# Kernel tuning notes

Measured on AMD Instinct MI355X. Metric: run time of the kernel, lower is better.

The kernel has to match this reference:

```python
import jax, jax.numpy as jnp
import numpy as np

B = 131072
EPS = 1e-5

def _attn(x, Wq, Wk, Wv, Wo):
    # x: (B, 10, 1); Wq/Wk/Wv: (1, 16); Wo: (16, 1)
    Q = x @ Wq  # (B, 10, 16)
    K = x @ Wk
    V = x @ Wv
    A = jnp.einsum('bqd,bkd->bqk', Q, K) / 4.0  # sqrt(16) = 4
    A = jax.nn.softmax(A, axis=1)  # NOTE: torch Softmax(dim=1) -> axis 1, not -1
    out = jnp.einsum('bqk,bkd->bqd', A, V) @ Wo  # (B, 10, 1)
    return out[..., 0]  # squeeze -> (B, 10)

def _bn(h, gamma, beta):
    # BatchNorm1d training-mode math (batch stats, biased variance)
    mu = jnp.mean(h, axis=0)
    var = jnp.mean(jnp.square(h - mu), axis=0)
    return gamma * (h - mu) * jax.lax.rsqrt(var + EPS) + beta

def setup_inputs() -> dict:
    key = jax.random.key(0)
    ks = jax.random.split(key, 24)
    n = lambda k, shp, s=1.0: (jax.random.normal(k, shp, dtype=jnp.float32) * s)
    inp = {
        'x':   n(ks[0], (B, 10, 1)),
        'Wq1': n(ks[1], (1, 16)), 'Wk1': n(ks[2], (1, 16)),
        'Wv1': n(ks[3], (1, 16)), 'Wo1': n(ks[4], (16, 1)),
        'Wq2': n(ks[5], (1, 16)), 'Wk2': n(ks[6], (1, 16)),
        'Wv2': n(ks[7], (1, 16)), 'Wo2': n(ks[8], (16, 1)),
        # layer1: Linear(10,128) BN ReLU Linear(128,256) BN ReLU Linear(256,10)
        'W1a': n(ks[9], (10, 128), 0.3), 'b1a': jnp.zeros((128,), jnp.float32),
        'g1a': jnp.ones((128,), jnp.float32), 'be1a': jnp.zeros((128,), jnp.float32),
        'W1b': n(ks[10], (128, 256), 0.09), 'b1b': jnp.zeros((256,), jnp.float32),
        'g1b': jnp.ones((256,), jnp.float32), 'be1b': jnp.zeros((256,), jnp.float32),
        'W1c': n(ks[11], (256, 10), 0.06), 'b1c': jnp.zeros((10,), jnp.float32),
        # layer2: Linear(10,128) BN ReLU Linear(128,256) BN ReLU Linear(256,2)
        'W2a': n(ks[12], (10, 128), 0.3), 'b2a': jnp.zeros((128,), jnp.float32),
        'g2a': jnp.ones((128,), jnp.float32), 'be2a': jnp.zeros((128,), jnp.float32),
        'W2b': n(ks[13], (128, 256), 0.09), 'b2b': jnp.zeros((256,), jnp.float32),
        'g2b': jnp.ones((256,), jnp.float32), 'be2b': jnp.zeros((256,), jnp.float32),
        'W2c': n(ks[14], (256, 2), 0.06), 'b2c': jnp.zeros((2,), jnp.float32),
    }
    return inp

def reference(x, Wq1, Wk1, Wv1, Wo1, Wq2, Wk2, Wv2, Wo2,
              W1a, b1a, g1a, be1a, W1b, b1b, g1b, be1b, W1c, b1c,
              W2a, b2a, g2a, be2a, W2b, b2b, g2b, be2b, W2c, b2c):
    h = _attn(x, Wq1, Wk1, Wv1, Wo1)                 # (B, 10)
    h = jax.nn.relu(_bn(h @ W1a + b1a, g1a, be1a))   # (B, 128)
    h = jax.nn.relu(_bn(h @ W1b + b1b, g1b, be1b))   # (B, 256)
    h = h @ W1c + b1c                                # (B, 10)
    h = _attn(h[..., None], Wq2, Wk2, Wv2, Wo2)      # (B, 10)
    h = jax.nn.relu(_bn(h @ W2a + b2a, g2a, be2a))   # (B, 128)
    h = jax.nn.relu(_bn(h @ W2b + b2b, g2b, be2b))   # (B, 256)
    return h @ W2c + b2c                             # (B, 2)
```

## Files before the change

### kernel.cpp

```cpp
#include <hip/hip_runtime.h>
#include <hip/hip_bf16.h>

#define EPS 1e-5f
constexpr int BN = 131072;
constexpr int NBKT = 32;

typedef __attribute__((ext_vector_type(8))) short bf16x8;
typedef __attribute__((ext_vector_type(4))) float f32x4;

constexpr size_t OFF_H   = 0;
constexpr size_t OFF_HH  = OFF_H  + (size_t)BN*10;
constexpr size_t OFF_M1  = OFF_HH + (size_t)BN*10;
constexpr size_t OFF_S2  = OFF_M1 + 65;
constexpr size_t OFF_M3  = OFF_S2 + 512;
constexpr size_t OFF_S4  = OFF_M3 + 65;
constexpr size_t OFF_WA1 = OFF_S4 + 512;
constexpr size_t OFF_BA1 = OFF_WA1 + 1280;
constexpr size_t OFF_WA2 = OFF_BA1 + 128;
constexpr size_t OFF_BA2 = OFF_WA2 + 1280;
constexpr size_t OFF_SC2 = OFF_BA2 + 128;
constexpr size_t OFF_TC2 = OFF_SC2 + 256;
constexpr size_t OFF_SC4 = OFF_TC2 + 256;
constexpr size_t OFF_TC4 = OFF_SC4 + 256;
constexpr size_t OFF_WB1 = OFF_TC4 + 256;
constexpr size_t OFF_BB1 = OFF_WB1 + 32768;
constexpr size_t OFF_WB2 = OFF_BB1 + 256;
constexpr size_t OFF_BB2 = OFF_WB2 + 32768;
constexpr size_t OFF_P1  = OFF_BB2 + 256;
constexpr size_t OFF_P3  = OFF_P1 + 512*65;
constexpr size_t OFF_S2B = OFF_P3 + 512*65;
constexpr size_t OFF_S4B = OFF_S2B + (size_t)NBKT*512;
constexpr size_t OFF_WT1 = OFF_S4B + (size_t)NBKT*512;
constexpr size_t OFF_WT2 = OFF_WT1 + 16384;
constexpr size_t OFF_END = OFF_WT2 + 16384;
constexpr size_t OFF_Z_BYTES = ((OFF_END*4 + 255) & ~(size_t)255);
constexpr size_t WS_NEED_OLD  = OFF_Z_BYTES + (size_t)BN*256*2;
constexpr size_t WS_NEED_MFMA = WS_NEED_OLD;

__device__ __forceinline__ float wsum(float v){
  v += __shfl_down(v, 32);
  v += __shfl_down(v, 16);
  v += __shfl_down(v, 8);
  v += __shfl_down(v, 4);
  v += __shfl_down(v, 2);
  v += __shfl_down(v, 1);
  return v;
}

__device__ __forceinline__ unsigned pk_bf16(float a, float b){
  union { __hip_bfloat16 h[2]; unsigned u; } cv;
  cv.h[0] = __float2bfloat16(a);
  cv.h[1] = __float2bfloat16(b);
  return cv.u;
}

__device__ __forceinline__ unsigned short bf16_1(float a){
  union { __hip_bfloat16 h; unsigned short u; } cv;
  cv.h = __float2bfloat16(a);
  return cv.u;
}

__device__ __forceinline__ void attn10(const float* xr, float cqk, float cvo, float* y){
  #pragma unroll
  for (int q=0;q<10;q++) y[q] = 0.f;
  #pragma unroll
  for (int k=0;k<10;k++){
    float t = cqk * xr[k];
    float m = t*xr[0];
    #pragma unroll
    for (int q=1;q<10;q++) m = fmaxf(m, t*xr[q]);
    float ex[10]; float s = 0.f;
    #pragma unroll
    for (int q=0;q<10;q++){ ex[q] = __expf(t*xr[q]-m); s += ex[q]; }
    float f = xr[k]/s;
    #pragma unroll
    for (int q=0;q<10;q++) y[q] += ex[q]*f;
  }
  #pragma unroll
  for (int q=0;q<10;q++) y[q] *= cvo;
}

__device__ __forceinline__ void moments_block(const float* y, float (*red)[65],
                                              float* Pb, int t){
  int lane = t & 63, w = t >> 6;
  #pragma unroll
  for (int i=0;i<10;i++){
    float v = wsum(y[i]);
    if (lane==0) red[w][i] = v;
  }
  #pragma unroll
  for (int i=0;i<10;i++){
    #pragma unroll
    for (int j=i;j<10;j++){
      float v = wsum(y[i]*y[j]);
      if (lane==0) red[w][10 + 10*i - i*(i-1)/2 + (j-i)] = v;
    }
  }
  __syncthreads();
  if (t < 65)
    Pb[(size_t)blockIdx.x*65 + t] = red[0][t]+red[1][t]+red[2][t]+red[3][t];
}

__device__ __forceinline__ void moments10(const float* y, float* M, int lane){
  #pragma unroll
  for (int i=0;i<10;i++){
    float s = wsum(y[i]);
    if (lane==0) atomicAdd(&M[i], s);
  }
  #pragma unroll
  for (int i=0;i<10;i++){
    #pragma unroll
    for (int j=i;j<10;j++){
      int id = 10*i - i*(i-1)/2 + (j-i);
      float s = wsum(y[i]*y[j]);
      if (lane==0) atomicAdd(&M[10+id], s);
    }
  }
}

__global__ __launch_bounds__(256) void k_attn_in(
    const float* __restrict__ x,
    const float* __restrict__ Wq, const float* __restrict__ Wk,
    const float* __restrict__ Wv, const float* __restrict__ Wo,
    float* __restrict__ h, float* __restrict__ Pb){
  __shared__ float red[4][65];
  int t = threadIdx.x;
  size_t b = (size_t)blockIdx.x*256 + t;
  float cqk=0.f, cvo=0.f;
  #pragma unroll
  for (int d=0;d<16;d++){ cqk += Wq[d]*Wk[d]; cvo += Wv[d]*Wo[d]; }
  cqk *= 0.25f;
  float xr[10];
  #pragma unroll
  for (int q=0;q<10;q++) xr[q] = x[b*10+q];
  float y[10];
  attn10(xr, cqk, cvo, y);
  #pragma unroll
  for (int q=0;q<10;q++) h[b*10+q] = y[q];
  moments_block(y, red, Pb, t);
}

__global__ void k_fold10_part(const float* __restrict__ Pb,
                              const float* __restrict__ W,
                              const float* __restrict__ bv, const float* __restrict__ g,
                              const float* __restrict__ be,
                              float* __restrict__ WT, float* __restrict__ bo){
  __shared__ float sM[65];
  int t = threadIdx.x;
  if (t < 65){
    float acc = 0.f;
    for (int gg=0; gg<512; gg++) acc += Pb[(size_t)gg*65 + t];
    sM[t] = acc;
  }
  __syncthreads();
  int j = t;
  if (j >= 128) return;
  const float invB = 1.f/(float)BN;
  float Eh[10];
  #pragma unroll
  for (int i=0;i<10;i++) Eh[i] = sM[i]*invB;
  float wj[10];
  #pragma unroll
  for (int i=0;i<10;i++) wj[i] = W[i*128+j];
  float mu = bv[j];
  #pragma unroll
  for (int i=0;i<10;i++) mu += Eh[i]*wj[i];
  float var = 0.f;
  #pragma unroll
  for (int i=0;i<10;i++){
    #pragma unroll
    for (int l=0;l<10;l++){
      int a = i<l ? i : l, c = i<l ? l : i;
      int id = 10*a - a*(a-1)/2 + (c-a);
      float cov = sM[10+id]*invB - Eh[i]*Eh[l];
      var += wj[i]*wj[l]*cov;
    }
  }
  float s = g[j]*rsqrtf(var + EPS);
  #pragma unroll
  for (int i=0;i<10;i++) WT[j*10+i] = wj[i]*s;
  bo[j] = (bv[j]-mu)*s + be[j];
}

__global__ void k_fold10_atomic(const float* __restrict__ M,
                                const float* __restrict__ W,
                                const float* __restrict__ bv, const float* __restrict__ g,
                                const float* __restrict__ be,
                                float* __restrict__ WT, float* __restrict__ bo){
  int j = threadIdx.x;
  if (j >= 128) return;
  const float invB = 1.f/(float)BN;
  float Eh[10];
  #pragma unroll
  for (int i=0;i<10;i++) Eh[i] = M[i]*invB;
  float wj[10];
  #pragma unroll
  for (int i=0;i<10;i++) wj[i] = W[i*128+j];
  float mu = bv[j];
  #pragma unroll
  for (int i=0;i<10;i++) mu += Eh[i]*wj[i];
  float var = 0.f;
  #pragma unroll
  for (int i=0;i<10;i++){
    #pragma unroll
    for (int l=0;l<10;l++){
      int a = i<l ? i : l, c = i<l ? l : i;
      int id = 10*a - a*(a-1)/2 + (c-a);
      float cov = M[10+id]*invB - Eh[i]*Eh[l];
      var += wj[i]*wj[l]*cov;
    }
  }
  float s = g[j]*rsqrtf(var + EPS);
  #pragma unroll
  for (int i=0;i<10;i++) WT[j*10+i] = wj[i]*s;
  bo[j] = (bv[j]-mu)*s + be[j];
}

__global__ void k_fold_affine(const float* __restrict__ stats,
                              const float* __restrict__ g,
                              const float* __restrict__ be,
                              float* __restrict__ s, float* __restrict__ tt){
  int j = threadIdx.x;
  if (j >= 256) return;
  float su = 0.f, sq = 0.f;
  #pragma unroll 4
  for (int k=0;k<NBKT;k++){
    su += stats[k*512 + j];
    sq += stats[k*512 + 256 + j];
  }
  const float invB = 1.f/(float)BN;
  float mu  = su*invB;
  float var = sq*invB - mu*mu;
  float sc = g[j]*rsqrtf(var + EPS);
  s[j]  = sc;
  tt[j] = be[j] - mu*sc;
}

__global__ __launch_bounds__(256) void k_prep_wt(const float* __restrict__ W,
                                                 unsigned short* __restrict__ WT){
  int idx = blockIdx.x*256 + threadIdx.x;
  int c = idx >> 7, k = idx & 127;
  WT[idx] = bf16_1(W[k*256 + c]);
}

__global__ __launch_bounds__(256) void k_layer_mfma(
    const float* __restrict__ h,
    const float* __restrict__ WaT,
    const float* __restrict__ ba,
    const unsigned short* __restrict__ WT,
    const float* __restrict__ bb,
    unsigned short* __restrict__ z,
    float* __restrict__ stats)
{
  __shared__ unsigned short h1s[64*128];
  __shared__ float hs[64][10];
  __shared__ float sWaT[1280];
  __shared__ float sstats[512];
  int t = threadIdx.x;
  int lane = t & 63, w = t >> 6;
  int ci = lane & 15, g = lane >> 4;
  size_t row0 = (size_t)blockIdx.x * 64;

  bf16x8 bfr[4][4];
  #pragma unroll
  for (int nt=0; nt<4; nt++)
    #pragma unroll
    for (int kt=0; kt<4; kt++){
      union { uint4 u; bf16x8 v; } cv;
      cv.u = *(const uint4*)(WT + (size_t)(w*64 + nt*16 + ci)*128 + kt*32 + g*8);
      bfr[nt][kt] = cv.v;
    }

  for (int idx = t; idx < 640; idx += 256) hs[idx/10][idx%10] = h[row0*10 + idx];
  for (int idx = t; idx < 1280; idx += 256) sWaT[idx] = WaT[idx];
  __syncthreads();

  {
    int r = lane;
    int i0 = w * 32;
    float hr[10];
    #pragma unroll
    for (int l=0;l<10;l++) hr[l] = hs[r][l];
    #pragma unroll
    for (int j=0;j<4;j++){
      unsigned pk[4];
      #pragma unroll
      for (int q=0;q<4;q++){
        int i = i0 + j*8 + q*2;
        float v0 = ba[i], v1 = ba[i+1];
        #pragma unroll
        for (int l=0;l<10;l++){
          v0 = fmaf(hr[l], sWaT[i*10+l],     v0);
          v1 = fmaf(hr[l], sWaT[(i+1)*10+l], v1);
        }
        pk[q] = pk_bf16(fmaxf(v0,0.f), fmaxf(v1,0.f));
      }
      int byte = r*256 + (((i0 + j*8)*2) ^ ((r&7)<<4));
      *(uint4*)((char*)h1s + byte) = make_uint4(pk[0],pk[1],pk[2],pk[3]);
    }
  }
  __syncthreads();

  f32x4 acc[4][4];
  #pragma unroll
  for (int mt=0;mt<4;mt++)
    #pragma unroll
    for (int nt=0;nt<4;nt++)
      acc[mt][nt] = (f32x4){0.f,0.f,0.f,0.f};

  #pragma unroll
  for (int mt=0; mt<4; mt++){
    int r = mt*16 + ci;
    bf16x8 af[4];
    #pragma unroll
    for (int kt=0; kt<4; kt++){
      int byte = r*256 + ((kt*64 + g*16) ^ ((r&7)<<4));
      af[kt] = *(const bf16x8*)((const char*)h1s + byte);
    }
    #pragma unroll
    for (int nt=0; nt<4; nt++)
      #pragma unroll
      for (int kt=0; kt<4; kt++)
        acc[mt][nt] = __builtin_amdgcn_mfma_f32_16x16x32_bf16(
            af[kt], bfr[nt][kt], acc[mt][nt], 0, 0, 0);
  }

  float bbv[4];
  #pragma unroll
  for (int nt=0;nt<4;nt++) bbv[nt] = bb[w*64 + nt*16 + ci];
  float csum[4] = {0,0,0,0}, csq[4] = {0,0,0,0};
  #pragma unroll
  for (int mt=0; mt<4; mt++){
    #pragma unroll
    for (int nt=0; nt<4; nt++){
      #pragma unroll
      for (int j=0;j<4;j++){
        float zv = acc[mt][nt][j] + bbv[nt];
        int r = mt*16 + g*4 + j;
        int c = w*64 + nt*16 + ci;
        z[(row0 + r)*256 + c] = bf16_1(zv);
        csum[nt] += zv;
        csq[nt]  += zv*zv;
      }
    }
  }
  #pragma unroll
  for (int nt=0; nt<4; nt++){
    float s1 = csum[nt], s2 = csq[nt];
    s1 += __shfl_down(s1, 32); s1 += __shfl_down(s1, 16);
    s2 += __shfl_down(s2, 32); s2 += __shfl_down(s2, 16);
    if (lane < 16){
      sstats[w*64 + nt*16 + ci]       = s1;
      sstats[256 + w*64 + nt*16 + ci] = s2;
    }
  }
  __syncthreads();
  int bkt = blockIdx.x & (NBKT-1);
  atomicAdd(&stats[bkt*512 + t], sstats[t]);
  atomicAdd(&stats[bkt*512 + 256 + t], sstats[256+t]);
}

__global__ __launch_bounds__(256) void k_layer_big(
    const float* __restrict__ h,
    const float* __restrict__ WaT,
    const float* __restrict__ ba,
    const float* __restrict__ Wb,
    const float* __restrict__ bb,
    unsigned short* __restrict__ z,
    float* __restrict__ stats)
{
  __shared__ float h1T[128][68];
  __shared__ float hs[64][10];
  __shared__ float sWaT[1280];
  __shared__ float sstats[512];
  int t = threadIdx.x;
  size_t row0 = (size_t)blockIdx.x * 64;

  for (int idx = t; idx < 640; idx += 256) hs[idx/10][idx%10] = h[row0*10 + idx];
  for (int idx = t; idx < 1280; idx += 256) sWaT[idx] = WaT[idx];
  sstats[t] = 0.f; sstats[256+t] = 0.f;
  __syncthreads();
  {
    int r  = t & 63;
    int i0 = (t >> 6) * 32;
    float hr[10];
    #pragma unroll
    for (int l=0;l<10;l++) hr[l] = hs[r][l];
    for (int k=0;k<32;k++){
      int i = i0 + k;
      float v = ba[i];
      #pragma unroll
      for (int l=0;l<10;l++) v = fmaf(hr[l], sWaT[i*10+l], v);
      h1T[i][r] = fmaxf(v, 0.f);
    }
  }
  __syncthreads();
  int tx = t & 15;
  int ty = t >> 4;
  float acc[4][16];
  #pragma unroll
  for (int r=0;r<4;r++)
    #pragma unroll
    for (int c=0;c<16;c++) acc[r][c] = 0.f;
  const float* __restrict__ wrow = Wb + tx*16;
  for (int i=0;i<128;i++){
    const float4* wp = (const float4*)(wrow + (size_t)i*256);
    float wv[16];
    #pragma unroll
    for (int q=0;q<4;q++){
      float4 w = wp[q];
      wv[4*q+0]=w.x; wv[4*q+1]=w.y; wv[4*q+2]=w.z; wv[4*q+3]=w.w;
    }
    float4 av = *(const float4*)&h1T[i][ty*4];
    float a4[4] = {av.x, av.y, av.z, av.w};
    #pragma unroll
    for (int r=0;r<4;r++)
      #pragma unroll
      for (int c=0;c<16;c++)
        acc[r][c] = fmaf(a4[r], wv[c], acc[r][c]);
  }
  #pragma unroll
  for (int r=0;r<4;r++){
    unsigned p[8];
    #pragma unroll
    for (int q=0;q<8;q++){
      float z0 = acc[r][2*q]   + bb[tx*16 + 2*q];
      float z1 = acc[r][2*q+1] + bb[tx*16 + 2*q+1];
      acc[r][2*q]   = z0;
      acc[r][2*q+1] = z1;
      p[q] = pk_bf16(z0, z1);
    }
    uint4* zp = (uint4*)(z + (row0 + ty*4 + r)*256 + tx*16);
    zp[0] = make_uint4(p[0],p[1],p[2],p[3]);
    zp[1] = make_uint4(p[4],p[5],p[6],p[7]);
  }
  int lane = t & 63;
  #pragma unroll
  for (int c=0;c<16;c++){
    float s1 = acc[0][c]+acc[1][c]+acc[2][c]+acc[3][c];
    float q1 = acc[0][c]*acc[0][c]+acc[1][c]*acc[1][c]
             + acc[2][c]*acc[2][c]+acc[3][c]*acc[3][c];
    s1 += __shfl_down(s1, 32); s1 += __shfl_down(s1, 16);
    q1 += __shfl_down(q1, 32); q1 += __shfl_down(q1, 16);
    if (lane < 16){
      atomicAdd(&sstats[tx*16+c], s1);
      atomicAdd(&sstats[256+tx*16+c], q1);
    }
  }
  __syncthreads();
  int bkt = blockIdx.x & (NBKT-1);
  atomicAdd(&stats[bkt*512 + t], sstats[t]);
  atomicAdd(&stats[bkt*512 + 256 + t], sstats[256+t]);
}

__global__ __launch_bounds__(256) void k_consume_mid(
    const unsigned short* __restrict__ z,
    const float* __restrict__ s_g, const float* __restrict__ t_g,
    const float* __restrict__ Wc,  const float* __restrict__ bc,
    const float* __restrict__ Wq, const float* __restrict__ Wk,
    const float* __restrict__ Wv, const float* __restrict__ Wo,
    float* __restrict__ hh, float* __restrict__ Pb){
  __shared__ float sW[2560];
  __shared__ float ss[256], st[256];
  __shared__ float red[4][65];
  int t = threadIdx.x;
  for (int idx=t; idx<2560; idx+=256) sW[idx] = Wc[idx];
  ss[t] = s_g[t]; st[t] = t_g[t];
  __syncthreads();
  size_t b = (size_t)blockIdx.x*256 + t;
  float z3[10];
  #pragma unroll
  for (int l=0;l<10;l++) z3[l] = bc[l];
  const uint4* zr = (const uint4*)(z + b*256);
  for (int v=0; v<32; v++){
    uint4 pkt = zr[v];
    unsigned w4[4] = {pkt.x, pkt.y, pkt.z, pkt.w};
    #pragma unroll
    for (int q=0;q<4;q++){
      int j = v*8 + q*2;
      float f0 = __uint_as_float(w4[q] << 16);
      float f1 = __uint_as_float(w4[q] & 0xffff0000u);
      float h20 = fmaxf(fmaf(ss[j],   f0, st[j]),   0.f);
      float h21 = fmaxf(fmaf(ss[j+1], f1, st[j+1]), 0.f);
      #pragma unroll
      for (int l=0;l<10;l++) z3[l] = fmaf(h20, sW[j*10+l], z3[l]);
      #pragma unroll
      for (int l=0;l<10;l++) z3[l] = fmaf(h21, sW[(j+1)*10+l], z3[l]);
    }
  }
  float cqk=0.f, cvo=0.f;
  #pragma unroll
  for (int d=0;d<16;d++){ cqk += Wq[d]*Wk[d]; cvo += Wv[d]*Wo[d]; }
  cqk *= 0.25f;
  float y[10];
  attn10(z3, cqk, cvo, y);
  #pragma unroll
  for (int q=0;q<10;q++) hh[b*10+q] = y[q];
  moments_block(y, red, Pb, t);
}

__global__ __launch_bounds__(256) void k_consume_out(
    const unsigned short* __restrict__ z,
    const float* __restrict__ s_g, const float* __restrict__ t_g,
    const float* __restrict__ Wc,  const float* __restrict__ bc,
    float* __restrict__ out){
  __shared__ float sW0[256], sW1[256], ss[256], st[256];
  int t = threadIdx.x;
  sW0[t] = Wc[t*2]; sW1[t] = Wc[t*2+1];
  ss[t] = s_g[t]; st[t] = t_g[t];
  __syncthreads();
  size_t b = (size_t)blockIdx.x*256 + t;
  float o0 = bc[0], o1 = bc[1];
  const uint4* zr = (const uint4*)(z + b*256);
  for (int v=0; v<32; v++){
    uint4 pkt = zr[v];
    unsigned w4[4] = {pkt.x, pkt.y, pkt.z, pkt.w};
    #pragma unroll
    for (int q=0;q<4;q++){
      int j = v*8 + q*2;
      float f0 = __uint_as_float(w4[q] << 16);
      float f1 = __uint_as_float(w4[q] & 0xffff0000u);
      float h20 = fmaxf(fmaf(ss[j],   f0, st[j]),   0.f);
      float h21 = fmaxf(fmaf(ss[j+1], f1, st[j+1]), 0.f);
      o0 = fmaf(h20, sW0[j],   o0); o1 = fmaf(h20, sW1[j],   o1);
      o0 = fmaf(h21, sW0[j+1], o0); o1 = fmaf(h21, sW1[j+1], o1);
    }
  }
  out[b*2]   = o0;
  out[b*2+1] = o1;
}

__global__ void k_fold_big(const float* __restrict__ stats,
                           const float* __restrict__ W,
                           const float* __restrict__ bv, const float* __restrict__ g,
                           const float* __restrict__ be,
                           float* __restrict__ Wf, float* __restrict__ bf){
  int j = blockIdx.x*256 + threadIdx.x;
  if (j >= 256) return;
  const float invB = 1.f/(float)BN;
  float mu  = stats[j]*invB;
  float var = stats[256+j]*invB - mu*mu;
  float s = g[j]*rsqrtf(var + EPS);
  bf[j] = (bv[j]-mu)*s + be[j];
  for (int i=0;i<128;i++) Wf[i*256+j] = W[i*256+j]*s;
}

__global__ __launch_bounds__(256) void k_mid(
    const float* __restrict__ h,
    const float* __restrict__ WaT, const float* __restrict__ ba,
    const float* __restrict__ Wb,  const float* __restrict__ bb,
    float* __restrict__ stats){
  int b = blockIdx.x*256 + threadIdx.x;
  if (b >= BN) return;
  float hr[10];
  #pragma unroll
  for (int l=0;l<10;l++) hr[l] = h[(size_t)b*10+l];
  int lane = threadIdx.x & 63;
  for (int jc=0;jc<4;jc++){
    float acc[64];
    #pragma unroll
    for (int j=0;j<64;j++) acc[j] = bb[jc*64+j];
    for (int i=0;i<128;i++){
      float h1 = ba[i];
      #pragma unroll
      for (int l=0;l<10;l++) h1 += hr[l]*WaT[i*10+l];
      h1 = fmaxf(h1, 0.f);
      const float* __restrict__ w = &Wb[i*256 + jc*64];
      #pragma unroll
      for (int j=0;j<64;j++) acc[j] += h1*w[j];
    }
    #pragma unroll
    for (int j=0;j<64;j++){
      float s1 = wsum(acc[j]);
      float s2 = wsum(acc[j]*acc[j]);
      if (lane==0){
        atomicAdd(&stats[jc*64+j], s1);
        atomicAdd(&stats[256+jc*64+j], s2);
      }
    }
  }
}

__global__ __launch_bounds__(256) void k_mid2(
    const float* __restrict__ h,
    const float* __restrict__ WaT, const float* __restrict__ ba,
    const float* __restrict__ Wbf, const float* __restrict__ bbf,
    const float* __restrict__ Wc,  const float* __restrict__ bc,
    const float* __restrict__ Wq, const float* __restrict__ Wk,
    const float* __restrict__ Wv, const float* __restrict__ Wo,
    float* __restrict__ hh, float* __restrict__ M){
  int b = blockIdx.x*256 + threadIdx.x;
  if (b >= BN) return;
  float hr[10];
  #pragma unroll
  for (int l=0;l<10;l++) hr[l] = h[(size_t)b*10+l];
  float z3[10];
  #pragma unroll
  for (int l=0;l<10;l++) z3[l] = bc[l];
  for (int jc=0;jc<4;jc++){
    float acc[64];
    #pragma unroll
    for (int j=0;j<64;j++) acc[j] = bbf[jc*64+j];
    for (int i=0;i<128;i++){
      float h1 = ba[i];
      #pragma unroll
      for (int l=0;l<10;l++) h1 += hr[l]*WaT[i*10+l];
      h1 = fmaxf(h1, 0.f);
      const float* __restrict__ w = &Wbf[i*256 + jc*64];
      #pragma unroll
      for (int j=0;j<64;j++) acc[j] += h1*w[j];
    }
    #pragma unroll
    for (int j=0;j<64;j++){
      float h2 = fmaxf(acc[j], 0.f);
      const float* __restrict__ wc = &Wc[(jc*64+j)*10];
      #pragma unroll
      for (int l=0;l<10;l++) z3[l] += h2*wc[l];
    }
  }
  float cqk=0.f, cvo=0.f;
  #pragma unroll
  for (int d=0;d<16;d++){ cqk += Wq[d]*Wk[d]; cvo += Wv[d]*Wo[d]; }
  cqk *= 0.25f;
  float y[10];
  attn10(z3, cqk, cvo, y);
  #pragma unroll
  for (int q=0;q<10;q++) hh[(size_t)b*10+q] = y[q];
  moments10(y, M, threadIdx.x & 63);
}

__global__ __launch_bounds__(256) void k_out(
    const float* __restrict__ h,
    const float* __restrict__ WaT, const float* __restrict__ ba,
    const float* __restrict__ Wbf, const float* __restrict__ bbf,
    const float* __restrict__ Wc,  const float* __restrict__ bc,
    float* __restrict__ out){
  int b = blockIdx.x*256 + threadIdx.x;
  if (b >= BN) return;
  float hr[10];
  #pragma unroll
  for (int l=0;l<10;l++) hr[l] = h[(size_t)b*10+l];
  float o0 = bc[0], o1 = bc[1];
  for (int jc=0;jc<4;jc++){
    float acc[64];
    #pragma unroll
    for (int j=0;j<64;j++) acc[j] = bbf[jc*64+j];
    for (int i=0;i<128;i++){
      float h4 = ba[i];
      #pragma unroll
      for (int l=0;l<10;l++) h4 += hr[l]*WaT[i*10+l];
      h4 = fmaxf(h4, 0.f);
      const float* __restrict__ w = &Wbf[i*256 + jc*64];
      #pragma unroll
      for (int j=0;j<64;j++) acc[j] += h4*w[j];
    }
    #pragma unroll
    for (int j=0;j<64;j++){
      float h5 = fmaxf(acc[j], 0.f);
      o0 += h5*Wc[(jc*64+j)*2];
      o1 += h5*Wc[(jc*64+j)*2+1];
    }
  }
  out[(size_t)b*2]   = o0;
  out[(size_t)b*2+1] = o1;
}

extern "C" void kernel_launch(void* const* d_in, const int* in_sizes, int n_in,
                              void* d_out, int out_size, void* d_ws, size_t ws_size,
                              hipStream_t stream){
  const float* x   = (const float*)d_in[0];
  const float* Wq1 = (const float*)d_in[1];
  const float* Wk1 = (const float*)d_in[2];
  const float* Wv1 = (const float*)d_in[3];
  const float* Wo1 = (const float*)d_in[4];
  const float* Wq2 = (const float*)d_in[5];
  const float* Wk2 = (const float*)d_in[6];
  const float* Wv2 = (const float*)d_in[7];
  const float* Wo2 = (const float*)d_in[8];
  const float* W1a = (const float*)d_in[9];  const float* b1a = (const float*)d_in[10];
  const float* g1a = (const float*)d_in[11]; const float* be1a= (const float*)d_in[12];
  const float* W1b = (const float*)d_in[13]; const float* b1b = (const float*)d_in[14];
  const float* g1b = (const float*)d_in[15]; const float* be1b= (const float*)d_in[16];
  const float* W1c = (const float*)d_in[17]; const float* b1c = (const float*)d_in[18];
  const float* W2a = (const float*)d_in[19]; const float* b2a = (const float*)d_in[20];
  const float* g2a = (const float*)d_in[21]; const float* be2a= (const float*)d_in[22];
  const float* W2b = (const float*)d_in[23]; const float* b2b = (const float*)d_in[24];
  const float* g2b = (const float*)d_in[25]; const float* be2b= (const float*)d_in[26];
  const float* W2c = (const float*)d_in[27]; const float* b2c = (const float*)d_in[28];

  float* f   = (float*)d_ws;
  float* h   = f + OFF_H;
  float* hh  = f + OFF_HH;
  float* M1  = f + OFF_M1;
  float* S2  = f + OFF_S2;
  float* M3  = f + OFF_M3;
  float* S4  = f + OFF_S4;
  float* WA1 = f + OFF_WA1; float* BA1 = f + OFF_BA1;
  float* WA2 = f + OFF_WA2; float* BA2 = f + OFF_BA2;
  float* SC2 = f + OFF_SC2; float* TC2 = f + OFF_TC2;
  float* SC4 = f + OFF_SC4; float* TC4 = f + OFF_TC4;
  float* WB1 = f + OFF_WB1; float* BB1 = f + OFF_BB1;
  float* WB2 = f + OFF_WB2; float* BB2 = f + OFF_BB2;
  float* P1  = f + OFF_P1;  float* P3  = f + OFF_P3;
  float* S2B = f + OFF_S2B; float* S4B = f + OFF_S4B;
  unsigned short* WT1 = (unsigned short*)(f + OFF_WT1);
  unsigned short* WT2 = (unsigned short*)(f + OFF_WT2);
  unsigned short* Z = (unsigned short*)((char*)d_ws + OFF_Z_BYTES);

  dim3 grid(BN/256), blk(256);

  if (ws_size >= WS_NEED_MFMA){
    hipMemsetAsync(S2B, 0, (size_t)2*NBKT*512*sizeof(float), stream);
    dim3 gbig(BN/64);
    k_prep_wt<<<128,blk,0,stream>>>(W1b, WT1);
    k_prep_wt<<<128,blk,0,stream>>>(W2b, WT2);
    k_attn_in<<<grid,blk,0,stream>>>(x, Wq1,Wk1,Wv1,Wo1, h, P1);
    k_fold10_part<<<1,128,0,stream>>>(P1, W1a,b1a,g1a,be1a, WA1,BA1);
    k_layer_mfma<<<gbig,blk,0,stream>>>(h, WA1,BA1, WT1,b1b, Z, S2B);
    k_fold_affine<<<1,256,0,stream>>>(S2B, g1b, be1b, SC2, TC2);
    k_consume_mid<<<grid,blk,0,stream>>>(Z, SC2,TC2, W1c,b1c, Wq2,Wk2,Wv2,Wo2, hh, P3);
    k_fold10_part<<<1,128,0,stream>>>(P3, W2a,b2a,g2a,be2a, WA2,BA2);
    k_layer_mfma<<<gbig,blk,0,stream>>>(hh, WA2,BA2, WT2,b2b, Z, S4B);
    k_fold_affine<<<1,256,0,stream>>>(S4B, g2b, be2b, SC4, TC4);
    k_consume_out<<<grid,blk,0,stream>>>(Z, SC4,TC4, W2c,b2c, (float*)d_out);
  } else {
    hipMemsetAsync(M1, 0, (65+512+65+512)*sizeof(float), stream);
    k_attn_in<<<grid,blk,0,stream>>>(x, Wq1,Wk1,Wv1,Wo1, h, P1);
    k_fold10_part<<<1,128,0,stream>>>(P1, W1a,b1a,g1a,be1a, WA1,BA1);
    k_mid<<<grid,blk,0,stream>>>(h, WA1,BA1, W1b,b1b, S2);
    k_fold_big<<<1,256,0,stream>>>(S2, W1b,b1b,g1b,be1b, WB1,BB1);
    k_mid2<<<grid,blk,0,stream>>>(h, WA1,BA1, WB1,BB1, W1c,b1c, Wq2,Wk2,Wv2,Wo2, hh, M3);
    k_fold10_atomic<<<1,128,0,stream>>>(M3, W2a,b2a,g2a,be2a, WA2,BA2);
    k_mid<<<grid,blk,0,stream>>>(hh, WA2,BA2, W2b,b2b, S4);
    k_fold_big<<<1,256,0,stream>>>(S4, W2b,b2b,g2b,be2b, WB2,BB2);
    k_out<<<grid,blk,0,stream>>>(hh, WA2,BA2, WB2,BB2, W2c,b2c, (float*)d_out);
  }
}
```

Baseline: 225.9 us.

## Store bf16 intermediate column-major and split consumer rows across thread pairs

Result: no change. 228.9 us (+1.3%).

```diff
diff --git a/kernel.cpp b/kernel.cpp
--- a/kernel.cpp
+++ b/kernel.cpp
@@ -27,15 +27,14 @@
 constexpr size_t OFF_WB2 = OFF_BB1 + 256;
 constexpr size_t OFF_BB2 = OFF_WB2 + 32768;
 constexpr size_t OFF_P1  = OFF_BB2 + 256;
-constexpr size_t OFF_P3  = OFF_P1 + 512*65;
-constexpr size_t OFF_S2B = OFF_P3 + 512*65;
+constexpr size_t OFF_P3  = OFF_P1 + 1024*65;
+constexpr size_t OFF_S2B = OFF_P3 + 1024*65;
 constexpr size_t OFF_S4B = OFF_S2B + (size_t)NBKT*512;
 constexpr size_t OFF_WT1 = OFF_S4B + (size_t)NBKT*512;
 constexpr size_t OFF_WT2 = OFF_WT1 + 16384;
 constexpr size_t OFF_END = OFF_WT2 + 16384;
 constexpr size_t OFF_Z_BYTES = ((OFF_END*4 + 255) & ~(size_t)255);
-constexpr size_t WS_NEED_OLD  = OFF_Z_BYTES + (size_t)BN*256*2;
-constexpr size_t WS_NEED_MFMA = WS_NEED_OLD;
+constexpr size_t WS_NEED = OFF_Z_BYTES + (size_t)256*BN*2;
 
 __device__ __forceinline__ float wsum(float v){
   v += __shfl_down(v, 32);
@@ -81,7 +80,7 @@
 }
 
 __device__ __forceinline__ void moments_block(const float* y, float (*red)[65],
-                                              float* Pb, int t){
+                                              float* Pb, int t, float scale){
   int lane = t & 63, w = t >> 6;
   #pragma unroll
   for (int i=0;i<10;i++){
@@ -98,7 +97,7 @@
   }
   __syncthreads();
   if (t < 65)
-    Pb[(size_t)blockIdx.x*65 + t] = red[0][t]+red[1][t]+red[2][t]+red[3][t];
+    Pb[(size_t)blockIdx.x*65 + t] = (red[0][t]+red[1][t]+red[2][t]+red[3][t])*scale;
 }
 
 __device__ __forceinline__ void moments10(const float* y, float* M, int lane){
@@ -123,34 +122,49 @@
     const float* __restrict__ Wq, const float* __restrict__ Wk,
     const float* __restrict__ Wv, const float* __restrict__ Wo,
     float* __restrict__ h, float* __restrict__ Pb){
+  __shared__ float xs[256][11];
   __shared__ float red[4][65];
   int t = threadIdx.x;
-  size_t b = (size_t)blockIdx.x*256 + t;
+  size_t base = (size_t)blockIdx.x*2560;
+  for (int idx=t; idx<2560; idx+=256) xs[idx/10][idx%10] = x[base+idx];
   float cqk=0.f, cvo=0.f;
   #pragma unroll
   for (int d=0;d<16;d++){ cqk += Wq[d]*Wk[d]; cvo += Wv[d]*Wo[d]; }
   cqk *= 0.25f;
+  __syncthreads();
   float xr[10];
   #pragma unroll
-  for (int q=0;q<10;q++) xr[q] = x[b*10+q];
+  for (int q=0;q<10;q++) xr[q] = xs[t][q];
   float y[10];
   attn10(xr, cqk, cvo, y);
   #pragma unroll
-  for (int q=0;q<10;q++) h[b*10+q] = y[q];
-  moments_block(y, red, Pb, t);
-}
-
-__global__ void k_fold10_part(const float* __restrict__ Pb,
+  for (int q=0;q<10;q++) xs[t][q] = y[q];
+  moments_block(y, red, Pb, t, 1.0f);
+  for (int idx=t; idx<2560; idx+=256) h[base+idx] = xs[idx/10][idx%10];
+}
+
+__global__ void k_fold10_part(const float* __restrict__ Pb, int npart,
                               const float* __restrict__ W,
                               const float* __restrict__ bv, const float* __restrict__ g,
                               const float* __restrict__ be,
                               float* __restrict__ WT, float* __restrict__ bo){
+  __shared__ float part[65][8];
   __shared__ float sM[65];
   int t = threadIdx.x;
+  if (t < 520){
+    int c = t>>3, k = t&7;
+    int n = npart>>3;
+    float acc = 0.f;
+    #pragma unroll 4
+    for (int i=0;i<n;i++) acc += Pb[(size_t)(k*n+i)*65 + c];
+    part[c][k] = acc;
+  }
+  __syncthreads();
   if (t < 65){
-    float acc = 0.f;
-    for (int gg=0; gg<512; gg++) acc += Pb[(size_t)gg*65 + t];
-    sM[t] = acc;
+    float a = 0.f;
+    #pragma unroll
+    for (int k=0;k<8;k++) a += part[t][k];
+    sM[t] = a;
   }
   __syncthreads();
   int j = t;
@@ -236,9 +250,13 @@
   tt[j] = be[j] - mu*sc;
 }
 
-__global__ __launch_bounds__(256) void k_prep_wt(const float* __restrict__ W,
-                                                 unsigned short* __restrict__ WT){
-  int idx = blockIdx.x*256 + threadIdx.x;
+__global__ __launch_bounds__(256) void k_prep_wt2(
+    const float* __restrict__ W1, const float* __restrict__ W2,
+    unsigned short* __restrict__ WT1, unsigned short* __restrict__ WT2){
+  int g = blockIdx.x;
+  const float* W = (g < 128) ? W1 : W2;
+  unsigned short* WT = (g < 128) ? WT1 : WT2;
+  int idx = (g & 127)*256 + threadIdx.x;
   int c = idx >> 7, k = idx & 127;
   WT[idx] = bf16_1(W[k*256 + c]);
 }
@@ -249,13 +267,14 @@
     const float* __restrict__ ba,
     const unsigned short* __restrict__ WT,
     const float* __restrict__ bb,
-    unsigned short* __restrict__ z,
+    unsigned short* __restrict__ zt,
     float* __restrict__ stats)
 {
-  __shared__ unsigned short h1s[64*128];
-  __shared__ float hs[64][10];
+  __shared__ unsigned short zs[256*72];
+  __shared__ float hs[64][11];
   __shared__ float sWaT[1280];
   __shared__ float sstats[512];
+  unsigned short* h1s = zs;
   int t = threadIdx.x;
   int lane = t & 63, w = t >> 6;
   int ci = lane & 15, g = lane >> 4;
@@ -330,20 +349,16 @@
   for (int nt=0;nt<4;nt++) bbv[nt] = bb[w*64 + nt*16 + ci];
   float csum[4] = {0,0,0,0}, csq[4] = {0,0,0,0};
   #pragma unroll
-  for (int mt=0; mt<4; mt++){
-    #pragma unroll
-    for (int nt=0; nt<4; nt++){
+  for (int mt=0; mt<4; mt++)
+    #pragma unroll
+    for (int nt=0; nt<4; nt++)
       #pragma unroll
       for (int j=0;j<4;j++){
         float zv = acc[mt][nt][j] + bbv[nt];
-        int r = mt*16 + g*4 + j;
-        int c = w*64 + nt*16 + ci;
-        z[(row0 + r)*256 + c] = bf16_1(zv);
+        acc[mt][nt][j] = zv;
         csum[nt] += zv;
         csq[nt]  += zv*zv;
       }
-    }
-  }
   #pragma unroll
   for (int nt=0; nt<4; nt++){
     float s1 = csum[nt], s2 = csq[nt];
@@ -358,103 +373,31 @@
   int bkt = blockIdx.x & (NBKT-1);
   atomicAdd(&stats[bkt*512 + t], sstats[t]);
   atomicAdd(&stats[bkt*512 + 256 + t], sstats[256+t]);
-}
-
-__global__ __launch_bounds__(256) void k_layer_big(
-    const float* __restrict__ h,
-    const float* __restrict__ WaT,
-    const float* __restrict__ ba,
-    const float* __restrict__ Wb,
-    const float* __restrict__ bb,
-    unsigned short* __restrict__ z,
-    float* __restrict__ stats)
-{
-  __shared__ float h1T[128][68];
-  __shared__ float hs[64][10];
-  __shared__ float sWaT[1280];
-  __shared__ float sstats[512];
-  int t = threadIdx.x;
-  size_t row0 = (size_t)blockIdx.x * 64;
-
-  for (int idx = t; idx < 640; idx += 256) hs[idx/10][idx%10] = h[row0*10 + idx];
-  for (int idx = t; idx < 1280; idx += 256) sWaT[idx] = WaT[idx];
-  sstats[t] = 0.f; sstats[256+t] = 0.f;
-  __syncthreads();
-  {
-    int r  = t & 63;
-    int i0 = (t >> 6) * 32;
-    float hr[10];
-    #pragma unroll
-    for (int l=0;l<10;l++) hr[l] = hs[r][l];
-    for (int k=0;k<32;k++){
-      int i = i0 + k;
-      float v = ba[i];
-      #pragma unroll
-      for (int l=0;l<10;l++) v = fmaf(hr[l], sWaT[i*10+l], v);
-      h1T[i][r] = fmaxf(v, 0.f);
-    }
-  }
-  __syncthreads();
-  int tx = t & 15;
-  int ty = t >> 4;
-  float acc[4][16];
-  #pragma unroll
-  for (int r=0;r<4;r++)
-    #pragma unroll
-    for (int c=0;c<16;c++) acc[r][c] = 0.f;
-  const float* __restrict__ wrow = Wb + tx*16;
-  for (int i=0;i<128;i++){
-    const float4* wp = (const float4*)(wrow + (size_t)i*256);
-    float wv[16];
-    #pragma unroll
-    for (int q=0;q<4;q++){
-      float4 w = wp[q];
-      wv[4*q+0]=w.x; wv[4*q+1]=w.y; wv[4*q+2]=w.z; wv[4*q+3]=w.w;
-    }
-    float4 av = *(const float4*)&h1T[i][ty*4];
-    float a4[4] = {av.x, av.y, av.z, av.w};
-    #pragma unroll
-    for (int r=0;r<4;r++)
-      #pragma unroll
-      for (int c=0;c<16;c++)
-        acc[r][c] = fmaf(a4[r], wv[c], acc[r][c]);
-  }
-  #pragma unroll
-  for (int r=0;r<4;r++){
-    unsigned p[8];
-    #pragma unroll
-    for (int q=0;q<8;q++){
-      float z0 = acc[r][2*q]   + bb[tx*16 + 2*q];
-      float z1 = acc[r][2*q+1] + bb[tx*16 + 2*q+1];
-      acc[r][2*q]   = z0;
-      acc[r][2*q+1] = z1;
-      p[q] = pk_bf16(z0, z1);
-    }
-    uint4* zp = (uint4*)(z + (row0 + ty*4 + r)*256 + tx*16);
-    zp[0] = make_uint4(p[0],p[1],p[2],p[3]);
-    zp[1] = make_uint4(p[4],p[5],p[6],p[7]);
-  }
-  int lane = t & 63;
-  #pragma unroll
-  for (int c=0;c<16;c++){
-    float s1 = acc[0][c]+acc[1][c]+acc[2][c]+acc[3][c];
-    float q1 = acc[0][c]*acc[0][c]+acc[1][c]*acc[1][c]
-             + acc[2][c]*acc[2][c]+acc[3][c]*acc[3][c];
-    s1 += __shfl_down(s1, 32); s1 += __shfl_down(s1, 16);
-    q1 += __shfl_down(q1, 32); q1 += __shfl_down(q1, 16);
-    if (lane < 16){
-      atomicAdd(&sstats[tx*16+c], s1);
-      atomicAdd(&sstats[256+tx*16+c], q1);
-    }
-  }
-  __syncthreads();
-  int bkt = blockIdx.x & (NBKT-1);
-  atomicAdd(&stats[bkt*512 + t], sstats[t]);
-  atomicAdd(&stats[bkt*512 + 256 + t], sstats[256+t]);
+
+  #pragma unroll
+  for (int mt=0; mt<4; mt++)
+    #pragma unroll
+    for (int nt=0; nt<4; nt++){
+      int c = w*64 + nt*16 + ci;
+      int r0 = mt*16 + g*4;
+      uint2 v;
+      v.x = pk_bf16(acc[mt][nt][0], acc[mt][nt][1]);
+      v.y = pk_bf16(acc[mt][nt][2], acc[mt][nt][3]);
+      *(uint2*)&zs[c*72 + r0] = v;
+    }
+  __syncthreads();
+
+  #pragma unroll
+  for (int pass=0; pass<8; pass++){
+    int c  = (t>>3) + pass*32;
+    int rc = (t&7)*8;
+    uint4 v = *(const uint4*)&zs[c*72 + rc];
+    *(uint4*)(zt + (size_t)c*BN + row0 + rc) = v;
+  }
 }
 
 __global__ __launch_bounds__(256) void k_consume_mid(
-    const unsigned short* __restrict__ z,
+    const unsigned short* __restrict__ zt,
     const float* __restrict__ s_g, const float* __restrict__ t_g,
     const float* __restrict__ Wc,  const float* __restrict__ bc,
     const float* __restrict__ Wq, const float* __restrict__ Wk,
@@ -463,44 +406,44 @@
   __shared__ float sW[2560];
   __shared__ float ss[256], st[256];
   __shared__ float red[4][65];
+  __shared__ float hhs[128][11];
   int t = threadIdx.x;
   for (int idx=t; idx<2560; idx+=256) sW[idx] = Wc[idx];
   ss[t] = s_g[t]; st[t] = t_g[t];
   __syncthreads();
-  size_t b = (size_t)blockIdx.x*256 + t;
+  int r = t >> 1, p = t & 1;
+  size_t b = (size_t)blockIdx.x*128 + r;
   float z3[10];
   #pragma unroll
-  for (int l=0;l<10;l++) z3[l] = bc[l];
-  const uint4* zr = (const uint4*)(z + b*256);
-  for (int v=0; v<32; v++){
-    uint4 pkt = zr[v];
-    unsigned w4[4] = {pkt.x, pkt.y, pkt.z, pkt.w};
-    #pragma unroll
-    for (int q=0;q<4;q++){
-      int j = v*8 + q*2;
-      float f0 = __uint_as_float(w4[q] << 16);
-      float f1 = __uint_as_float(w4[q] & 0xffff0000u);
-      float h20 = fmaxf(fmaf(ss[j],   f0, st[j]),   0.f);
-      float h21 = fmaxf(fmaf(ss[j+1], f1, st[j+1]), 0.f);
-      #pragma unroll
-      for (int l=0;l<10;l++) z3[l] = fmaf(h20, sW[j*10+l], z3[l]);
-      #pragma unroll
-      for (int l=0;l<10;l++) z3[l] = fmaf(h21, sW[(j+1)*10+l], z3[l]);
-    }
-  }
+  for (int l=0;l<10;l++) z3[l] = p ? 0.f : bc[l];
+  int c0 = p*128;
+  #pragma unroll 4
+  for (int c=c0; c<c0+128; c++){
+    unsigned short u = zt[(size_t)c*BN + b];
+    float f = __uint_as_float(((unsigned)u) << 16);
+    float h2 = fmaxf(fmaf(ss[c], f, st[c]), 0.f);
+    #pragma unroll
+    for (int l=0;l<10;l++) z3[l] = fmaf(h2, sW[c*10+l], z3[l]);
+  }
+  #pragma unroll
+  for (int l=0;l<10;l++) z3[l] += __shfl_xor(z3[l], 1);
   float cqk=0.f, cvo=0.f;
   #pragma unroll
   for (int d=0;d<16;d++){ cqk += Wq[d]*Wk[d]; cvo += Wv[d]*Wo[d]; }
   cqk *= 0.25f;
   float y[10];
   attn10(z3, cqk, cvo, y);
-  #pragma unroll
-  for (int q=0;q<10;q++) hh[b*10+q] = y[q];
-  moments_block(y, red, Pb, t);
+  if (!p){
+    #pragma unroll
+    for (int q=0;q<10;q++) hhs[r][q] = y[q];
+  }
+  moments_block(y, red, Pb, t, 0.5f);
+  for (int idx=t; idx<1280; idx+=256)
+    hh[(size_t)blockIdx.x*1280 + idx] = hhs[idx/10][idx%10];
 }
 
 __global__ __launch_bounds__(256) void k_consume_out(
-    const unsigned short* __restrict__ z,
+    const unsigned short* __restrict__ zt,
     const float* __restrict__ s_g, const float* __restrict__ t_g,
     const float* __restrict__ Wc,  const float* __restrict__ bc,
     float* __restrict__ out){
@@ -509,25 +452,22 @@
   sW0[t] = Wc[t*2]; sW1[t] = Wc[t*2+1];
   ss[t] = s_g[t]; st[t] = t_g[t];
   __syncthreads();
-  size_t b = (size_t)blockIdx.x*256 + t;
-  float o0 = bc[0], o1 = bc[1];
-  const uint4* zr = (const uint4*)(z + b*256);
-  for (int v=0; v<32; v++){
-    uint4 pkt = zr[v];
-    unsigned w4[4] = {pkt.x, pkt.y, pkt.z, pkt.w};
-    #pragma unroll
-    for (int q=0;q<4;q++){
-      int j = v*8 + q*2;
-      float f0 = __uint_as_float(w4[q] << 16);
-      float f1 = __uint_as_float(w4[q] & 0xffff0000u);
-      float h20 = fmaxf(fmaf(ss[j],   f0, st[j]),   0.f);
-      float h21 = fmaxf(fmaf(ss[j+1], f1, st[j+1]), 0.f);
-      o0 = fmaf(h20, sW0[j],   o0); o1 = fmaf(h20, sW1[j],   o1);
-      o0 = fmaf(h21, sW0[j+1], o0); o1 = fmaf(h21, sW1[j+1], o1);
-    }
-  }
-  out[b*2]   = o0;
-  out[b*2+1] = o1;
+  int r = t >> 1, p = t & 1;
+  size_t b = (size_t)blockIdx.x*128 + r;
+  float o0 = p ? 0.f : bc[0];
+  float o1 = p ? 0.f : bc[1];
+  int c0 = p*128;
+  #pragma unroll 4
+  for (int c=c0; c<c0+128; c++){
+    unsigned short u = zt[(size_t)c*BN + b];
+    float f = __uint_as_float(((unsigned)u) << 16);
+    float h5 = fmaxf(fmaf(ss[c], f, st[c]), 0.f);
+    o0 = fmaf(h5, sW0[c], o0);
+    o1 = fmaf(h5, sW1[c], o1);
+  }
+  o0 += __shfl_xor(o0, 1);
+  o1 += __shfl_xor(o1, 1);
+  out[b*2 + p] = p ? o1 : o0;
 }
 
 __global__ void k_fold_big(const float* __restrict__ stats,
@@ -705,34 +645,37 @@
   float* S2B = f + OFF_S2B; float* S4B = f + OFF_S4B;
   unsigned short* WT1 = (unsigned short*)(f + OFF_WT1);
   unsigned short* WT2 = (unsigned short*)(f + OFF_WT2);
-  unsigned short* Z = (unsigned short*)((char*)d_ws + OFF_Z_BYTES);
-
-  dim3 grid(BN/256), blk(256);
-
-  if (ws_size >= WS_NEED_MFMA){
+  unsigned short* ZT = (unsigned short*)((char*)d_ws + OFF_Z_BYTES);
+
+  dim3 blk(256);
+  dim3 grid256(BN/256);
+  dim3 grid128(BN/128);
+  dim3 grid64(BN/64);
+
+  if (ws_size >= WS_NEED){
     hipMemsetAsync(S2B, 0, (size_t)2*NBKT*512*sizeof(float), stream);
-    dim3 gbig(BN/64);
-    k_prep_wt<<<128,blk,0,stream>>>(W1b, WT1);
-    k_prep_wt<<<128,blk,0,stream>>>(W2b, WT2);
-    k_attn_in<<<grid,blk,0,stream>>>(x, Wq1,Wk1,Wv1,Wo1, h, P1);
-    k_fold10_part<<<1,128,0,stream>>>(P1, W1a,b1a,g1a,be1a, WA1,BA1);
-    k_layer_mfma<<<gbig,blk,0,stream>>>(h, WA1,BA1, WT1,b1b, Z, S2B);
+    k_prep_wt2<<<256,blk,0,stream>>>(W1b, W2b, WT1, WT2);
+    k_attn_in<<<grid256,blk,0,stream>>>(x, Wq1,Wk1,Wv1,Wo1, h, P1);
+    k_fold10_part<<<1,576,0,stream>>>(P1, 512, W1a,b1a,g1a,be1a, WA1,BA1);
+    k_layer_mfma<<<grid64,blk,0,stream>>>(h, WA1,BA1, WT1,b1b, ZT, S2B);
     k_fold_affine<<<1,256,0,stream>>>(S2B, g1b, be1b, SC2, TC2);
-    k_consume_mid<<<grid,blk,0,stream>>>(Z, SC2,TC2, W1c,b1c, Wq2,Wk2,Wv2,Wo2, hh, P3);
-    k_fold10_part<<<1,128,0,stream>>>(P3, W2a,b2a,g2a,be2a, WA2,BA2);
-    k_layer_mfma<<<gbig,blk,0,stream>>>(hh, WA2,BA2, WT2,b2b, Z, S4B);
+    k_consume_mid<<<grid128,blk,0,stream>>>(ZT, SC2,TC2, W1c,b1c,
+                                            Wq2,Wk2,Wv2,Wo2, hh, P3);
+    k_fold10_part<<<1,576,0,stream>>>(P3, 1024, W2a,b2a,g2a,be2a, WA2,BA2);
+    k_layer_mfma<<<grid64,blk,0,stream>>>(hh, WA2,BA2, WT2,b2b, ZT, S4B);
     k_fold_affine<<<1,256,0,stream>>>(S4B, g2b, be2b, SC4, TC4);
-    k_consume_out<<<grid,blk,0,stream>>>(Z, SC4,TC4, W2c,b2c, (float*)d_out);
+    k_consume_out<<<grid128,blk,0,stream>>>(ZT, SC4,TC4, W2c,b2c, (float*)d_out);
   } else {
     hipMemsetAsync(M1, 0, (65+512+65+512)*sizeof(float), stream);
-    k_attn_in<<<grid,blk,0,stream>>>(x, Wq1,Wk1,Wv1,Wo1, h, P1);
-    k_fold10_part<<<1,128,0,stream>>>(P1, W1a,b1a,g1a,be1a, WA1,BA1);
-    k_mid<<<grid,blk,0,stream>>>(h, WA1,BA1, W1b,b1b, S2);
+    k_attn_in<<<grid256,blk,0,stream>>>(x, Wq1,Wk1,Wv1,Wo1, h, P1);
+    k_fold10_part<<<1,576,0,stream>>>(P1, 512, W1a,b1a,g1a,be1a, WA1,BA1);
+    k_mid<<<grid256,blk,0,stream>>>(h, WA1,BA1, W1b,b1b, S2);
     k_fold_big<<<1,256,0,stream>>>(S2, W1b,b1b,g1b,be1b, WB1,BB1);
-    k_mid2<<<grid,blk,0,stream>>>(h, WA1,BA1, WB1,BB1, W1c,b1c, Wq2,Wk2,Wv2,Wo2, hh, M3);
+    k_mid2<<<grid256,blk,0,stream>>>(h, WA1,BA1, WB1,BB1, W1c,b1c,
+                                     Wq2,Wk2,Wv2,Wo2, hh, M3);
     k_fold10_atomic<<<1,128,0,stream>>>(M3, W2a,b2a,g2a,be2a, WA2,BA2);
-    k_mid<<<grid,blk,0,stream>>>(hh, WA2,BA2, W2b,b2b, S4);
+    k_mid<<<grid256,blk,0,stream>>>(hh, WA2,BA2, W2b,b2b, S4);
     k_fold_big<<<1,256,0,stream>>>(S4, W2b,b2b,g2b,be2b, WB2,BB2);
-    k_out<<<grid,blk,0,stream>>>(hh, WA2,BA2, WB2,BB2, W2c,b2c, (float*)d_out);
-  }
-}
+    k_out<<<grid256,blk,0,stream>>>(hh, WA2,BA2, WB2,BB2, W2c,b2c, (float*)d_out);
+  }
+}
```
